# Kernel optimization log

Hardware: AMD Instinct MI355X
Metric: run time of the kernel (lower is better)

Reference implementation:

```python
import jax, jax.numpy as jnp
import numpy as np

T, H = 2048, 1024
NH, NKV, HD = 8, 2, 128
E, TOPK, NG, TKG = 16, 4, 4, 2
F, FS = 1024, 1024
EPS = 1e-6
ROUTED_SCALE = 2.0
THETA = 10000.0


def _rmsnorm(x, w):
    return x * jax.lax.rsqrt(jnp.mean(x * x, axis=-1, keepdims=True) + EPS) * w


def setup_inputs() -> dict:
    key = jax.random.key(0)
    ks = jax.random.split(key, 12)
    s = 0.02
    return {
        "hidden_states": jax.random.normal(ks[0], (T, H), jnp.float32),
        "residual": jax.random.normal(ks[1], (T, H), jnp.float32),
        "position_ids": jnp.arange(T, dtype=jnp.int32),
        "ln1_w": jnp.ones((H,), jnp.float32),
        "qkv_w": s * jax.random.normal(ks[2], (H, (NH + 2 * NKV) * HD), jnp.float32),
        "qnorm_w": jnp.ones((HD,), jnp.float32),
        "knorm_w": jnp.ones((HD,), jnp.float32),
        "dense_w": s * jax.random.normal(ks[3], (NH * HD, H), jnp.float32),
        "ln2_w": jnp.ones((H,), jnp.float32),
        "gate_w": s * jax.random.normal(ks[4], (H, E), jnp.float32),
        "expert_bias": 0.1 * jax.random.normal(ks[5], (E,), jnp.float32),
        "w13": s * jax.random.normal(ks[6], (E, H, 2 * F), jnp.float32),
        "w2": s * jax.random.normal(ks[7], (E, F, H), jnp.float32),
        "ws_gate_up": s * jax.random.normal(ks[8], (H, 2 * FS), jnp.float32),
        "ws_down": s * jax.random.normal(ks[9], (FS, H), jnp.float32),
    }


def block_forward(hidden_states, residual, position_ids, ln1_w, qkv_w, qnorm_w,
                  knorm_w, dense_w, ln2_w, gate_w, expert_bias, w13, w2,
                  ws_gate_up, ws_down):
    # fused add + RMSNorm (input_layernorm with residual)
    resid = hidden_states + residual
    h = _rmsnorm(resid, ln1_w)

    # --- attention ---
    qkv = h @ qkv_w  # [T, (NH+2*NKV)*HD]
    q = qkv[:, : NH * HD].reshape(T, NH, HD)
    k = qkv[:, NH * HD : (NH + NKV) * HD].reshape(T, NKV, HD)
    v = qkv[:, (NH + NKV) * HD :].reshape(T, NKV, HD)
    q = _rmsnorm(q, qnorm_w)  # qk-norm per head_dim
    k = _rmsnorm(k, knorm_w)

    # neox-style RoPE over full head_dim
    inv_freq = 1.0 / (THETA ** (jnp.arange(0, HD, 2, dtype=jnp.float32) / HD))
    ang = position_ids.astype(jnp.float32)[:, None] * inv_freq[None, :]  # [T, HD/2]
    cos = jnp.cos(ang)[:, None, :]
    sin = jnp.sin(ang)[:, None, :]

    def rope(x):
        x1, x2 = x[..., : HD // 2], x[..., HD // 2 :]
        return jnp.concatenate([x1 * cos - x2 * sin, x2 * cos + x1 * sin], axis=-1)

    q, k = rope(q), rope(k)
    rep = NH // NKV
    kr = jnp.repeat(k, rep, axis=1)  # [T, NH, HD]
    vr = jnp.repeat(v, rep, axis=1)

    scores = jnp.einsum("qhd,khd->hqk", q, kr) * (HD ** -0.5)
    causal = jnp.tril(jnp.ones((T, T), bool))
    scores = jnp.where(causal[None], scores, jnp.finfo(scores.dtype).min)
    probs = jax.nn.softmax(scores, axis=-1)
    ctx = jnp.einsum("hqk,khd->qhd", probs, vr).reshape(T, NH * HD)
    attn_out = ctx @ dense_w

    # fused add + RMSNorm (post_attention_layernorm)
    resid2 = attn_out + resid
    h2 = _rmsnorm(resid2, ln2_w)

    # --- MoE router: sigmoid scoring + correction bias, grouped top-k ---
    logits = h2.astype(jnp.float32) @ gate_w  # router in fp32
    s_scores = jax.nn.sigmoid(logits)  # [T, E]
    sfc = s_scores + expert_bias[None, :]
    gview = sfc.reshape(T, NG, E // NG)
    gscores = jax.lax.top_k(gview, 2)[0].sum(-1)  # sum of top-2 per group
    gidx = jax.lax.top_k(gscores, TKG)[1]  # [T, TKG]
    gmask = jax.nn.one_hot(gidx, NG, dtype=sfc.dtype).sum(1)  # [T, NG]
    smask = jnp.repeat(gmask, E // NG, axis=1)  # [T, E]
    masked = jnp.where(smask > 0, sfc, -jnp.inf)
    topk_idx = jax.lax.top_k(masked, TOPK)[1]  # [T, TOPK]
    topk_w = jnp.take_along_axis(s_scores, topk_idx, axis=1)  # weights w/o bias
    topk_w = topk_w / (topk_w.sum(-1, keepdims=True) + 1e-20)  # renormalize
    combine = (jax.nn.one_hot(topk_idx, E, dtype=topk_w.dtype) * topk_w[..., None]).sum(1)  # [T, E]

    # routed experts (dense-over-experts reference for the grouped GEMM)
    gu = jnp.einsum("th,ehf->tef", h2, w13)  # [T, E, 2F]
    g, u = gu[..., :F], gu[..., F:]
    act = jax.nn.silu(g) * u
    y = jnp.einsum("tef,efh->teh", act, w2)
    routed = jnp.einsum("teh,te->th", y, combine) * ROUTED_SCALE

    # shared expert (SwiGLU MLP)
    su = h2 @ ws_gate_up
    shared = (jax.nn.silu(su[:, :FS]) * su[:, FS:]) @ ws_down

    mlp_out = routed + shared
    return mlp_out, resid2


def reference(hidden_states, residual, position_ids, ln1_w, qkv_w, qnorm_w,
              knorm_w, dense_w, ln2_w, gate_w, expert_bias, w13, w2,
              ws_gate_up, ws_down):
    return block_forward(hidden_states, residual, position_ids, ln1_w, qkv_w,
                         qnorm_w, knorm_w, dense_w, ln2_w, gate_w, expert_bias,
                         w13, w2, ws_gate_up, ws_down)
```

## Files before the change

kernel.cpp:

```cpp
#include <hip/hip_runtime.h>
#include <hip/hip_bf16.h>


#define T_TOK 2048
#define H_DIM 1024
#define NHEAD 8
#define NKVH 2
#define HDIM 128
#define QKV_DIM 1536
#define E_EXP 16
#define TOPKE 4
#define F_DIM 1024
#define FS_DIM 1024
#define NPAIR (T_TOK*TOPKE)
#define EPS_F 1e-6f

#define DEV __device__ __forceinline__

typedef __attribute__((ext_vector_type(4))) float f32x4;
typedef __attribute__((ext_vector_type(8))) short s16x8;

DEV float us2f(unsigned short u){ return __uint_as_float(((unsigned int)u)<<16); }
DEV unsigned short f2us(float f){
  __hip_bfloat16 b = __float2bfloat16(f);
  unsigned short u; __builtin_memcpy(&u,&b,2); return u;
}

DEV void gl2lds16(const void* g, void* l){
  __builtin_amdgcn_global_load_lds(
      (const __attribute__((address_space(1))) void*)g,
      (__attribute__((address_space(3))) void*)l, 16, 0, 0);
}

DEV float bred_sum(float v, float* sm){
  #pragma unroll
  for(int o=32;o>0;o>>=1) v += __shfl_down(v,o);
  int w = threadIdx.x>>6, l = threadIdx.x&63;
  __syncthreads();
  if(l==0) sm[w]=v;
  __syncthreads();
  return sm[0]+sm[1]+sm[2]+sm[3];
}

__global__ __launch_bounds__(256) void k_cvt_t(const float* __restrict__ in,
    unsigned short* __restrict__ out, int Kd, int Nd){
  const int z = blockIdx.z;
  const int kb = blockIdx.y*32, nb = blockIdx.x*32;
  __shared__ float Lt[32][33];
  const int tid = threadIdx.x;
  const int r = tid>>3, c4 = (tid&7)*4;
  const float* src = in + (long long)z*Kd*Nd + (long long)(kb+r)*Nd + nb + c4;
  float4 v = *(const float4*)src;
  Lt[r][c4+0]=v.x; Lt[r][c4+1]=v.y; Lt[r][c4+2]=v.z; Lt[r][c4+3]=v.w;
  __syncthreads();
  ushort4 o;
  o.x = f2us(Lt[c4+0][r]); o.y = f2us(Lt[c4+1][r]);
  o.z = f2us(Lt[c4+2][r]); o.w = f2us(Lt[c4+3][r]);
  *(ushort4*)(out + (long long)z*Nd*Kd + (long long)(nb+r)*Kd + kb + c4) = o;
}

template<bool GROUPED, bool GATHER>
__global__ __launch_bounds__(256) void gemm_mfma(
    const unsigned short* __restrict__ A, int lda,
    const unsigned short* __restrict__ Bt, int ldbt, long long bstride,
    unsigned short* __restrict__ C, int ldc,
    const int* __restrict__ rowidx, const int* __restrict__ grpoff,
    int Mdense, int K){
  const int z = blockIdx.z;
  const int rb = GROUPED ? grpoff[z] : 0;
  const int re = GROUPED ? grpoff[z+1] : Mdense;
  const int m0 = rb + blockIdx.y*128;
  if(m0 >= re) return;
  const int n0 = blockIdx.x*128;
  const unsigned short* Bz = Bt + (long long)z*bstride;

  __shared__ unsigned short As[128][32];
  __shared__ unsigned short Bs[128][32];

  const int tid = threadIdx.x;
  const int s0 = tid, s1 = tid+256;
  int gr0 = m0 + (s0>>2), gr1 = m0 + (s1>>2);
  if(GROUPED){ gr0 = min(gr0, re-1); gr1 = min(gr1, re-1); }
  if(GATHER){ gr0 = rowidx[gr0]; gr1 = rowidx[gr1]; }
  const unsigned short* ag0 = A + (long long)gr0*lda + (s0&3)*8;
  const unsigned short* ag1 = A + (long long)gr1*lda + (s1&3)*8;
  const unsigned short* bg0 = Bz + (long long)(n0 + (s0>>2))*ldbt + (s0&3)*8;
  const unsigned short* bg1 = Bz + (long long)(n0 + (s1>>2))*ldbt + (s1&3)*8;
  char* asb = (char*)&As[0][0];
  char* bsb = (char*)&Bs[0][0];
  const int wb = (tid & 192)*16;

  const int w = tid>>6, lane = tid&63;
  const int wm = (w>>1)*64, wn = (w&1)*64;
  const int fr = lane&15, q8 = (lane>>4)*8;

  f32x4 zero = {0.f,0.f,0.f,0.f};
  f32x4 acc[4][4];
  #pragma unroll
  for(int mi=0;mi<4;mi++)
    #pragma unroll
    for(int ni=0;ni<4;ni++) acc[mi][ni]=zero;

  for(int k0=0;k0<K;k0+=32){
    __syncthreads();
    gl2lds16(ag0 + k0, asb + wb);
    gl2lds16(ag1 + k0, asb + 4096 + wb);
    gl2lds16(bg0 + k0, bsb + wb);
    gl2lds16(bg1 + k0, bsb + 4096 + wb);
    __syncthreads();
    s16x8 af[4], bf[4];
    #pragma unroll
    for(int mi=0;mi<4;mi++) af[mi] = *(const s16x8*)&As[wm+mi*16+fr][q8];
    #pragma unroll
    for(int ni=0;ni<4;ni++) bf[ni] = *(const s16x8*)&Bs[wn+ni*16+fr][q8];
    #pragma unroll
    for(int mi=0;mi<4;mi++)
      #pragma unroll
      for(int ni=0;ni<4;ni++)
        acc[mi][ni] = __builtin_amdgcn_mfma_f32_16x16x32_bf16(af[mi], bf[ni], acc[mi][ni], 0,0,0);
  }
  const int q4 = (lane>>4)*4;
  #pragma unroll
  for(int mi=0;mi<4;mi++)
    #pragma unroll
    for(int ni=0;ni<4;ni++){
      const int col = n0 + wn + ni*16 + fr;
      #pragma unroll
      for(int r=0;r<4;r++){
        const int row = m0 + wm + mi*16 + q4 + r;
        if(row < re) C[(long long)row*ldc + col] = f2us(acc[mi][ni][r]);
      }
    }
}

__global__ __launch_bounds__(256) void k_silu(const unsigned short* __restrict__ gu,
    unsigned short* __restrict__ act){
  const int r = blockIdx.x, c = threadIdx.x*4;
  const ushort4 g4 = *(const ushort4*)(gu + (long long)r*2048 + c);
  const ushort4 u4 = *(const ushort4*)(gu + (long long)r*2048 + 1024 + c);
  float g[4] = {us2f(g4.x),us2f(g4.y),us2f(g4.z),us2f(g4.w)};
  float u[4] = {us2f(u4.x),us2f(u4.y),us2f(u4.z),us2f(u4.w)};
  ushort4 o;
  o.x = f2us((g[0]/(1.f+__expf(-g[0])))*u[0]);
  o.y = f2us((g[1]/(1.f+__expf(-g[1])))*u[1]);
  o.z = f2us((g[2]/(1.f+__expf(-g[2])))*u[2]);
  o.w = f2us((g[3]/(1.f+__expf(-g[3])))*u[3]);
  *(ushort4*)(act + (long long)r*1024 + c) = o;
}

__global__ __launch_bounds__(256) void k_add_rmsnorm(const float* __restrict__ hs,
    const float* __restrict__ rs, const float* __restrict__ w,
    float* __restrict__ resid, float* __restrict__ h){
  int t = blockIdx.x, tid = threadIdx.x;
  __shared__ float sm[4];
  const long base = (long)t*H_DIM;
  float x[4]; float ss = 0.f;
  #pragma unroll
  for(int i=0;i<4;i++){
    int c = tid + i*256;
    float v = hs[base+c] + rs[base+c];
    x[i]=v; resid[base+c]=v; ss += v*v;
  }
  float tot = bred_sum(ss, sm);
  float rms = rsqrtf(tot/(float)H_DIM + EPS_F);
  #pragma unroll
  for(int i=0;i<4;i++){
    int c = tid + i*256;
    h[base+c] = x[i]*rms*w[c];
  }
}

template<int EPI_ADD>
__global__ __launch_bounds__(256) void gemm_f32(
    const float* __restrict__ A, int lda,
    const float* __restrict__ B, int ldb,
    float* __restrict__ C, int ldc,
    const float* __restrict__ D, int M, int K){
  const int m0 = blockIdx.y*128;
  const int n0 = blockIdx.x*64;
  __shared__ float As[16][132];
  __shared__ float Bs[16][65];
  float acc[8][4];
  #pragma unroll
  for(int i=0;i<8;i++)
    #pragma unroll
    for(int j=0;j<4;j++) acc[i][j]=0.f;
  const int tid = threadIdx.x;
  const int tx = tid & 15, ty = tid >> 4;
  const int ar = tid >> 1, ac = (tid & 1)*8;
  const int brr = tid >> 4, bc = (tid & 15)*4;
  const float* Aptr = A + (long long)(m0+ar)*lda;
  for(int k0=0;k0<K;k0+=16){
    float4 a0 = *(const float4*)(Aptr + k0 + ac);
    float4 a1 = *(const float4*)(Aptr + k0 + ac + 4);
    float4 bv = *(const float4*)(B + (long long)(k0+brr)*ldb + n0 + bc);
    __syncthreads();
    As[ac+0][ar]=a0.x; As[ac+1][ar]=a0.y; As[ac+2][ar]=a0.z; As[ac+3][ar]=a0.w;
    As[ac+4][ar]=a1.x; As[ac+5][ar]=a1.y; As[ac+6][ar]=a1.z; As[ac+7][ar]=a1.w;
    Bs[brr][bc+0]=bv.x; Bs[brr][bc+1]=bv.y; Bs[brr][bc+2]=bv.z; Bs[brr][bc+3]=bv.w;
    __syncthreads();
    #pragma unroll
    for(int kk=0;kk<16;kk++){
      float a[8], b[4];
      #pragma unroll
      for(int i=0;i<8;i++) a[i]=As[kk][ty*8+i];
      #pragma unroll
      for(int j=0;j<4;j++) b[j]=Bs[kk][tx*4+j];
      #pragma unroll
      for(int i=0;i<8;i++)
        #pragma unroll
        for(int j=0;j<4;j++) acc[i][j] = fmaf(a[i], b[j], acc[i][j]);
    }
  }
  #pragma unroll
  for(int i=0;i<8;i++){
    int r = m0 + ty*8 + i;
    float* crow = C + (long long)r*ldc + n0 + tx*4;
    float4 v = make_float4(acc[i][0],acc[i][1],acc[i][2],acc[i][3]);
    if(EPI_ADD){
      const float4 d = *(const float4*)(D + (long long)r*ldc + n0 + tx*4);
      v.x+=d.x; v.y+=d.y; v.z+=d.z; v.w+=d.w;
    }
    *(float4*)crow = v;
  }
}

__global__ __launch_bounds__(64) void k_qkv_post(const float* __restrict__ qkv,
    const float* __restrict__ qw, const float* __restrict__ kw,
    const int* __restrict__ pos,
    float* __restrict__ qb, float* __restrict__ kb, float* __restrict__ vb){
  int slot = blockIdx.x, t = blockIdx.y, lane = threadIdx.x;
  const float* x = qkv + (long long)t*QKV_DIM + slot*HDIM;
  float x0 = x[lane], x1 = x[lane+64];
  if(slot < 10){
    float ss = x0*x0 + x1*x1;
    #pragma unroll
    for(int o=32;o>0;o>>=1) ss += __shfl_xor(ss,o);
    float rms = rsqrtf(ss/(float)HDIM + EPS_F);
    const float* w = (slot<8)? qw : kw;
    float n0 = x0*rms*w[lane];
    float n1 = x1*rms*w[lane+64];
    float p = (float)pos[t];
    float invf = __expf(-((float)lane/64.f)*9.210340371976184f);
    float ang = p*invf;
    float s = sinf(ang), c = cosf(ang);
    float o0 = n0*c - n1*s;
    float o1 = n1*c + n0*s;
    float* dst = (slot<8)? (qb + ((long long)slot*T_TOK + t)*HDIM)
                         : (kb + ((long long)(slot-8)*T_TOK + t)*HDIM);
    dst[lane]=o0; dst[lane+64]=o1;
  } else {
    float* dst = vb + ((long long)(slot-10)*T_TOK + t)*HDIM;
    dst[lane]=x0; dst[lane+64]=x1;
  }
}

#define FBQ 32
#define FBK 64
__global__ __launch_bounds__(256,2) void k_flash(const float* __restrict__ qb,
    const float* __restrict__ kb, const float* __restrict__ vb,
    float* __restrict__ ctx){
  const int h = blockIdx.x;
  const int by = blockIdx.y;
  const int qt = (by < 32) ? (63 - by) : (by - 32);
  const int kv = h >> 2;
  const int q0 = qt * FBQ;
  const int tid = threadIdx.x;
  const int tx = tid & 15, ty = tid >> 4;
  __shared__ float Qs[HDIM][32];
  __shared__ float Ks[HDIM][64];
  __shared__ float Vs[FBK][HDIM];
  const float scale = 0.08838834764831845f;

  {
    int r = tid>>3, cb = (tid&7)*16;
    const float* src = qb + ((long long)h*T_TOK + q0 + r)*HDIM + cb;
    #pragma unroll
    for(int j=0;j<4;j++){
      float4 v4 = *(const float4*)(src + j*4);
      Qs[cb+j*4+0][r]=v4.x; Qs[cb+j*4+1][r]=v4.y;
      Qs[cb+j*4+2][r]=v4.z; Qs[cb+j*4+3][r]=v4.w;
    }
  }

  float m0=-1e30f, m1=-1e30f, l0=0.f, l1=0.f;
  float O0[8], O1[8];
  #pragma unroll
  for(int j=0;j<8;j++){ O0[j]=0.f; O1[j]=0.f; }

  const int nkt = (qt>>1) + 1;
  const float* kbase = kb + (long long)kv*T_TOK*HDIM;
  const float* vbase = vb + (long long)kv*T_TOK*HDIM;
  const int lbase = tid & 48;

  for(int kt=0; kt<nkt; kt++){
    const int k0 = kt*FBK;
    __syncthreads();
    {
      int r = tid>>2, cb = (tid&3)*32;
      const float* ks = kbase + (long long)(k0+r)*HDIM + cb;
      #pragma unroll
      for(int j=0;j<8;j++){
        float4 v4 = *(const float4*)(ks + j*4);
        Ks[cb+j*4+0][r]=v4.x; Ks[cb+j*4+1][r]=v4.y;
        Ks[cb+j*4+2][r]=v4.z; Ks[cb+j*4+3][r]=v4.w;
      }
      #pragma unroll
      for(int j=0;j<8;j++){
        int idx = tid + 256*j;
        int vr = idx>>5, dc = (idx&31)*4;
        *(float4*)&Vs[vr][dc] = *(const float4*)(vbase + (long long)(k0+vr)*HDIM + dc);
      }
    }
    __syncthreads();

    float s00=0,s01=0,s02=0,s03=0, s10=0,s11=0,s12=0,s13=0;
    const float* qsp = &Qs[0][ty*2];
    const float* ksp = &Ks[0][tx*4];
    #pragma unroll 8
    for(int kk=0;kk<HDIM;kk++){
      float2 q2 = *(const float2*)(qsp + kk*32);
      float4 k4 = *(const float4*)(ksp + kk*64);
      s00=fmaf(q2.x,k4.x,s00); s01=fmaf(q2.x,k4.y,s01);
      s02=fmaf(q2.x,k4.z,s02); s03=fmaf(q2.x,k4.w,s03);
      s10=fmaf(q2.y,k4.x,s10); s11=fmaf(q2.y,k4.y,s11);
      s12=fmaf(q2.y,k4.z,s12); s13=fmaf(q2.y,k4.w,s13);
    }
    float p0[4] = {s00*scale, s01*scale, s02*scale, s03*scale};
    float p1[4] = {s10*scale, s11*scale, s12*scale, s13*scale};
    if(kt == nkt-1){
      #pragma unroll
      for(int ci=0;ci<4;ci++){
        int c = k0 + tx*4 + ci;
        if(c > q0 + ty*2)     p0[ci] = -1e30f;
        if(c > q0 + ty*2 + 1) p1[ci] = -1e30f;
      }
    }
    float rm0 = fmaxf(fmaxf(p0[0],p0[1]),fmaxf(p0[2],p0[3]));
    float rm1 = fmaxf(fmaxf(p1[0],p1[1]),fmaxf(p1[2],p1[3]));
    #pragma unroll
    for(int o=1;o<16;o<<=1){
      rm0 = fmaxf(rm0, __shfl_xor(rm0,o));
      rm1 = fmaxf(rm1, __shfl_xor(rm1,o));
    }
    float mn0 = fmaxf(m0,rm0), mn1 = fmaxf(m1,rm1);
    float a0 = __expf(m0-mn0), a1 = __expf(m1-mn1);
    float rs0=0.f, rs1=0.f;
    #pragma unroll
    for(int ci=0;ci<4;ci++){
      p0[ci] = __expf(p0[ci]-mn0); rs0 += p0[ci];
      p1[ci] = __expf(p1[ci]-mn1); rs1 += p1[ci];
    }
    #pragma unroll
    for(int o=1;o<16;o<<=1){
      rs0 += __shfl_xor(rs0,o);
      rs1 += __shfl_xor(rs1,o);
    }
    l0 = l0*a0 + rs0; l1 = l1*a1 + rs1;
    m0 = mn0; m1 = mn1;
    #pragma unroll
    for(int j=0;j<8;j++){ O0[j]*=a0; O1[j]*=a1; }

    #pragma unroll 4
    for(int kc=0;kc<16;kc++){
      float pa[4], pb[4];
      #pragma unroll
      for(int ki=0;ki<4;ki++){
        pa[ki] = __shfl(p0[ki], lbase + kc);
        pb[ki] = __shfl(p1[ki], lbase + kc);
      }
      #pragma unroll
      for(int ki=0;ki<4;ki++){
        const float* vrow = &Vs[kc*4+ki][0];
        float4 va  = *(const float4*)(vrow + tx*4);
        float4 vb4 = *(const float4*)(vrow + 64 + tx*4);
        float qa = pa[ki], qb2 = pb[ki];
        O0[0]=fmaf(qa,va.x,O0[0]);  O0[1]=fmaf(qa,va.y,O0[1]);
        O0[2]=fmaf(qa,va.z,O0[2]);  O0[3]=fmaf(qa,va.w,O0[3]);
        O0[4]=fmaf(qa,vb4.x,O0[4]); O0[5]=fmaf(qa,vb4.y,O0[5]);
        O0[6]=fmaf(qa,vb4.z,O0[6]); O0[7]=fmaf(qa,vb4.w,O0[7]);
        O1[0]=fmaf(qb2,va.x,O1[0]);  O1[1]=fmaf(qb2,va.y,O1[1]);
        O1[2]=fmaf(qb2,va.z,O1[2]);  O1[3]=fmaf(qb2,va.w,O1[3]);
        O1[4]=fmaf(qb2,vb4.x,O1[4]); O1[5]=fmaf(qb2,vb4.y,O1[5]);
        O1[6]=fmaf(qb2,vb4.z,O1[6]); O1[7]=fmaf(qb2,vb4.w,O1[7]);
      }
    }
  }
  float inv0 = 1.f/l0, inv1 = 1.f/l1;
  float* dst0 = ctx + (long long)(q0 + ty*2)*(NHEAD*HDIM) + h*HDIM + tx*4;
  float* dst1 = dst0 + NHEAD*HDIM;
  *(float4*)dst0      = make_float4(O0[0]*inv0,O0[1]*inv0,O0[2]*inv0,O0[3]*inv0);
  *(float4*)(dst0+64) = make_float4(O0[4]*inv0,O0[5]*inv0,O0[6]*inv0,O0[7]*inv0);
  *(float4*)dst1      = make_float4(O1[0]*inv1,O1[1]*inv1,O1[2]*inv1,O1[3]*inv1);
  *(float4*)(dst1+64) = make_float4(O1[4]*inv1,O1[5]*inv1,O1[6]*inv1,O1[7]*inv1);
}

__global__ __launch_bounds__(256) void k_rms2(const float* __restrict__ r2,
    const float* __restrict__ w, float* __restrict__ h2f,
    unsigned short* __restrict__ h2b){
  int t = blockIdx.x, tid = threadIdx.x;
  __shared__ float sm[4];
  const long base = (long)t*H_DIM;
  float x[4]; float ss=0.f;
  #pragma unroll
  for(int i=0;i<4;i++){
    int c = tid+i*256;
    float v = r2[base+c];
    x[i]=v; ss += v*v;
  }
  float tot = bred_sum(ss, sm);
  float rms = rsqrtf(tot/(float)H_DIM + EPS_F);
  #pragma unroll
  for(int i=0;i<4;i++){
    int c = tid+i*256;
    float v = x[i]*rms*w[c];
    h2f[base+c] = v;
    h2b[base+c] = f2us(v);
  }
}

__global__ __launch_bounds__(256) void k_router(const float* __restrict__ h2,
    const float* __restrict__ gw, const float* __restrict__ eb,
    int* __restrict__ topk_idx, float* __restrict__ topk_w, int* __restrict__ counts){
  int t = blockIdx.x, tid = threadIdx.x;
  int e = tid & 15, seg = tid >> 4;
  const float* hrow = h2 + (long long)t*H_DIM;
  float part = 0.f;
  #pragma unroll 4
  for(int i=0;i<64;i++){
    int hh = seg*64 + i;
    part += hrow[hh]*gw[hh*E_EXP + e];
  }
  __shared__ float pm[16][17];
  __shared__ float sS[16], sfc[16];
  pm[seg][e] = part;
  __syncthreads();
  if(tid < 16){
    float l = 0.f;
    #pragma unroll
    for(int s=0;s<16;s++) l += pm[s][tid];
    float sg = 1.f/(1.f+expf(-l));
    sS[tid]=sg; sfc[tid]=sg+eb[tid];
  }
  __syncthreads();
  if(tid==0){
    float gs[4];
    #pragma unroll
    for(int g=0; g<4; g++){
      float m1=-1e30f, m2=-1e30f;
      for(int j=0;j<4;j++){
        float v=sfc[g*4+j];
        if(v>m1){ m2=m1; m1=v; } else if(v>m2){ m2=v; }
      }
      gs[g]=m1+m2;
    }
    int g1=0; for(int g=1;g<4;g++) if(gs[g]>gs[g1]) g1=g;
    int g2=-1; for(int g=0;g<4;g++){ if(g==g1) continue; if(g2<0||gs[g]>gs[g2]) g2=g; }
    bool taken[16];
    #pragma unroll
    for(int i=0;i<16;i++) taken[i]=false;
    int idx[4];
    for(int j=0;j<4;j++){
      int best=-1; float bv=-1e30f;
      for(int i=0;i<16;i++){
        int g=i>>2;
        if(g!=g1 && g!=g2) continue;
        if(taken[i]) continue;
        if(best<0 || sfc[i]>bv){ best=i; bv=sfc[i]; }
      }
      taken[best]=true; idx[j]=best;
    }
    float w[4]; float s=0.f;
    #pragma unroll
    for(int j=0;j<4;j++){ w[j]=sS[idx[j]]; s+=w[j]; }
    s += 1e-20f;
    #pragma unroll
    for(int j=0;j<4;j++){
      topk_idx[t*4+j]=idx[j];
      topk_w[t*4+j]=w[j]/s;
      atomicAdd(&counts[idx[j]],1);
    }
  }
}

__global__ void k_zero(int* __restrict__ counts){ if(threadIdx.x<16) counts[threadIdx.x]=0; }

__global__ void k_scan(const int* __restrict__ counts, int* __restrict__ offs, int* __restrict__ cursor){
  if(threadIdx.x==0){
    int s=0;
    for(int e2=0;e2<16;e2++){ offs[e2]=s; cursor[e2]=s; s+=counts[e2]; }
    offs[16]=s;
  }
}

__global__ __launch_bounds__(256) void k_scatter(const int* __restrict__ topk_idx,
    int* __restrict__ cursor, int* __restrict__ pair_tok, int* __restrict__ tok2pair){
  int i = blockIdx.x*256 + threadIdx.x;
  int e = topk_idx[i];
  int pos = atomicAdd(&cursor[e],1);
  pair_tok[pos] = i>>2;
  tok2pair[i] = pos;
}

__global__ __launch_bounds__(256) void k_combine(const unsigned short* __restrict__ y,
    const unsigned short* __restrict__ sout, const int* __restrict__ tok2pair,
    const float* __restrict__ topk_w, float* __restrict__ out0){
  int t = blockIdx.x, tid = threadIdx.x;
  int p[4]; float w[4];
  #pragma unroll
  for(int j=0;j<4;j++){ p[j]=tok2pair[t*4+j]; w[j]=topk_w[t*4+j]*2.0f; }
  const long base = (long)t*H_DIM;
  #pragma unroll
  for(int i=0;i<4;i++){
    int c = tid + i*256;
    float v = us2f(sout[base+c]);
    #pragma unroll
    for(int j=0;j<4;j++) v += w[j]*us2f(y[(long long)p[j]*H_DIM + c]);
    out0[base+c] = v;
  }
}

extern "C" void kernel_launch(void* const* d_in, const int* in_sizes, int n_in,
                              void* d_out, int out_size, void* d_ws, size_t ws_size,
                              hipStream_t stream) {
  const float* hs   = (const float*)d_in[0];
  const float* rsd  = (const float*)d_in[1];
  const int*   pos  = (const int*)d_in[2];
  const float* ln1  = (const float*)d_in[3];
  const float* qkvw = (const float*)d_in[4];
  const float* qnw  = (const float*)d_in[5];
  const float* knw  = (const float*)d_in[6];
  const float* dw   = (const float*)d_in[7];
  const float* ln2  = (const float*)d_in[8];
  const float* gw   = (const float*)d_in[9];
  const float* eb   = (const float*)d_in[10];
  const float* w13  = (const float*)d_in[11];
  const float* w2   = (const float*)d_in[12];
  const float* wsgu = (const float*)d_in[13];
  const float* wsd  = (const float*)d_in[14];
  float* out0 = (float*)d_out;
  float* out1 = out0 + (size_t)T_TOK*H_DIM;

  char* W = (char*)d_ws;
  float* resid = (float*)(W + 0);
  float* h     = (float*)(W + 8388608);
  float* ctx   = h;
  float* qkv   = (float*)(W + 16777216);
  float* qb    = (float*)(W + 29360128);
  float* h2f   = (float*)(W + 37748736);
  float* kb    = (float*)(W + 46137344);
  float* vb    = (float*)(W + 48234496);
  unsigned short* gu    = (unsigned short*)(W + 8388608);
  unsigned short* ybuf  = (unsigned short*)(W + 8388608);
  unsigned short* sgu   = (unsigned short*)(W + 16777216);
  unsigned short* sact  = (unsigned short*)(W + 0);
  unsigned short* sout  = (unsigned short*)(W + 46137344);
  unsigned short* h2b   = (unsigned short*)(W + 50331648);
  unsigned short* act   = (unsigned short*)(W + 54525952);
  unsigned short* w13t  = (unsigned short*)(W + 71303168);
  unsigned short* w2t   = (unsigned short*)(W + 138412032);
  unsigned short* wsgut = (unsigned short*)(W + 171966464);
  unsigned short* wsdt  = (unsigned short*)(W + 176160768);
  float* topkw = (float*)(W + 178257920);
  int* topki   = (int*)(W + 178290688);
  int* ptok    = (int*)(W + 178323456);
  int* t2p     = (int*)(W + 178356224);
  int* cnt     = (int*)(W + 178388992);
  int* offs    = (int*)(W + 178389056);
  int* cur     = (int*)(W + 178389184);

  k_cvt_t<<<dim3(64,32,16), 256, 0, stream>>>(w13,  w13t,  1024, 2048);
  k_cvt_t<<<dim3(32,32,16), 256, 0, stream>>>(w2,   w2t,   1024, 1024);
  k_cvt_t<<<dim3(64,32,1),  256, 0, stream>>>(wsgu, wsgut, 1024, 2048);
  k_cvt_t<<<dim3(32,32,1),  256, 0, stream>>>(wsd,  wsdt,  1024, 1024);
  k_add_rmsnorm<<<T_TOK, 256, 0, stream>>>(hs, rsd, ln1, resid, h);
  gemm_f32<0><<<dim3(QKV_DIM/64, T_TOK/128), 256, 0, stream>>>(
      h, H_DIM, qkvw, QKV_DIM, qkv, QKV_DIM, nullptr, T_TOK, H_DIM);
  k_qkv_post<<<dim3(12, T_TOK), 64, 0, stream>>>(qkv, qnw, knw, pos, qb, kb, vb);
  k_flash<<<dim3(NHEAD, 64), 256, 0, stream>>>(qb, kb, vb, ctx);
  gemm_f32<1><<<dim3(H_DIM/64, T_TOK/128), 256, 0, stream>>>(
      ctx, NHEAD*HDIM, dw, H_DIM, out1, H_DIM, resid, T_TOK, NHEAD*HDIM);
  k_rms2<<<T_TOK, 256, 0, stream>>>(out1, ln2, h2f, h2b);
  k_zero<<<1, 64, 0, stream>>>(cnt);
  k_router<<<T_TOK, 256, 0, stream>>>(h2f, gw, eb, topki, topkw, cnt);
  k_scan<<<1, 64, 0, stream>>>(cnt, offs, cur);
  k_scatter<<<NPAIR/256, 256, 0, stream>>>(topki, cur, ptok, t2p);
  gemm_mfma<false,false><<<dim3(16,16,1), 256, 0, stream>>>(
      h2b, 1024, wsgut, 1024, 0, sgu, 2048, nullptr, nullptr, T_TOK, 1024);
  k_silu<<<T_TOK, 256, 0, stream>>>(sgu, sact);
  gemm_mfma<false,false><<<dim3(8,16,1), 256, 0, stream>>>(
      sact, 1024, wsdt, 1024, 0, sout, 1024, nullptr, nullptr, T_TOK, 1024);
  gemm_mfma<true,true><<<dim3(16,64,16), 256, 0, stream>>>(
      h2b, 1024, w13t, 1024, (long long)2048*1024, gu, 2048, ptok, offs, 0, 1024);
  k_silu<<<NPAIR, 256, 0, stream>>>(gu, act);
  gemm_mfma<true,false><<<dim3(8,64,16), 256, 0, stream>>>(
      act, 1024, w2t, 1024, (long long)1024*1024, ybuf, 1024, nullptr, offs, 0, 1024);
  k_combine<<<T_TOK, 256, 0, stream>>>(ybuf, sout, t2p, topkw, out0);
}
```

Measured before the change: 1.107 ms.

## Restructure flash attention with 128-key tiles, swizzled async K staging, LDS-staged probabilities

Rewrites the causal attention kernel to process 128-key tiles, halving the outer iteration count. Each thread now computes a 4x4 score tile. K is staged into a swizzled shared-memory buffer with direct global-to-LDS copies. Q and V are read straight from global memory through the cache instead of shared memory. The softmax probabilities are written to a swizzled LDS region that reuses the tail of the K buffer, replacing the cross-lane shuffle broadcast. This aims to cut shuffle and LDS transpose overhead, at the cost of more global/L2 traffic for Q and V, a larger 64KB shared-memory footprint, and extra barriers.

After: 1.120 ms. Within noise of the previous version (+1.2%).

```diff
diff --git a/kernel.cpp b/kernel.cpp
--- a/kernel.cpp
+++ b/kernel.cpp
@@ -256,7 +256,7 @@
 }
 
 #define FBQ 32
-#define FBK 64
+#define FBK 128
 __global__ __launch_bounds__(256,2) void k_flash(const float* __restrict__ qb,
     const float* __restrict__ kb, const float* __restrict__ vb,
     float* __restrict__ ctx){
@@ -266,133 +266,145 @@
   const int kv = h >> 2;
   const int q0 = qt * FBQ;
   const int tid = threadIdx.x;
-  const int tx = tid & 15, ty = tid >> 4;
-  __shared__ float Qs[HDIM][32];
-  __shared__ float Ks[HDIM][64];
-  __shared__ float Vs[FBK][HDIM];
+  const int lane = tid & 63;
+  const int w = tid >> 6;
+  const int tx = tid & 31;
+  const int ty = tid >> 5;
+  const int fsw = tx & 7;
+
+  __shared__ float4 smem4[4096];
+  char*  smem = (char*)smem4;
+  float* Ksf  = (float*)smem;
+  float* Psf  = (float*)(smem + 49152);
+
   const float scale = 0.08838834764831845f;
-
-  {
-    int r = tid>>3, cb = (tid&7)*16;
-    const float* src = qb + ((long long)h*T_TOK + q0 + r)*HDIM + cb;
-    #pragma unroll
-    for(int j=0;j<4;j++){
-      float4 v4 = *(const float4*)(src + j*4);
-      Qs[cb+j*4+0][r]=v4.x; Qs[cb+j*4+1][r]=v4.y;
-      Qs[cb+j*4+2][r]=v4.z; Qs[cb+j*4+3][r]=v4.w;
-    }
-  }
-
-  float m0=-1e30f, m1=-1e30f, l0=0.f, l1=0.f;
-  float O0[8], O1[8];
-  #pragma unroll
-  for(int j=0;j<8;j++){ O0[j]=0.f; O1[j]=0.f; }
-
-  const int nkt = (qt>>1) + 1;
   const float* kbase = kb + (long long)kv*T_TOK*HDIM;
   const float* vbase = vb + (long long)kv*T_TOK*HDIM;
-  const int lbase = tid & 48;
+  const float* qrow0 = qb + ((long long)h*T_TOK + q0 + ty*4)*HDIM;
+
+  float m_[4], l_[4], O[4][4];
+  #pragma unroll
+  for(int qi=0;qi<4;qi++){
+    m_[qi] = -1e30f; l_[qi] = 0.f;
+    #pragma unroll
+    for(int j=0;j<4;j++) O[qi][j] = 0.f;
+  }
+
+  const int nkt = (qt >> 2) + 1;
 
   for(int kt=0; kt<nkt; kt++){
-    const int k0 = kt*FBK;
+    const int k0 = kt * FBK;
     __syncthreads();
     {
-      int r = tid>>2, cb = (tid&3)*32;
-      const float* ks = kbase + (long long)(k0+r)*HDIM + cb;
-      #pragma unroll
-      for(int j=0;j<8;j++){
-        float4 v4 = *(const float4*)(ks + j*4);
-        Ks[cb+j*4+0][r]=v4.x; Ks[cb+j*4+1][r]=v4.y;
-        Ks[cb+j*4+2][r]=v4.z; Ks[cb+j*4+3][r]=v4.w;
+      const float* kcur = kbase + (long long)k0*HDIM;
+      #pragma unroll
+      for(int i=0;i<16;i++){
+        const int rbase = (w<<5) + (i<<1);
+        const int f = (i>>1) & 7;
+        const float* src = kcur + (long long)(rbase + (lane>>5))*HDIM
+                                + (((lane&31)^f)<<2);
+        gl2lds16(src, smem + rbase*512);
       }
-      #pragma unroll
-      for(int j=0;j<8;j++){
-        int idx = tid + 256*j;
-        int vr = idx>>5, dc = (idx&31)*4;
-        *(float4*)&Vs[vr][dc] = *(const float4*)(vbase + (long long)(k0+vr)*HDIM + dc);
+    }
+    __syncthreads();
+
+    float s[4][4];
+    #pragma unroll
+    for(int qi=0;qi<4;qi++)
+      #pragma unroll
+      for(int ki=0;ki<4;ki++) s[qi][ki] = 0.f;
+
+    #pragma unroll 2
+    for(int dc=0; dc<32; dc++){
+      float4 qv[4];
+      #pragma unroll
+      for(int qi=0;qi<4;qi++) qv[qi] = *(const float4*)(qrow0 + qi*HDIM + dc*4);
+      float4 kf[4];
+      #pragma unroll
+      for(int ki=0;ki<4;ki++)
+        kf[ki] = *(const float4*)&Ksf[(size_t)(4*tx+ki)*128 + ((dc ^ fsw)<<2)];
+      #pragma unroll
+      for(int qi=0;qi<4;qi++)
+        #pragma unroll
+        for(int ki=0;ki<4;ki++){
+          s[qi][ki] = fmaf(qv[qi].x, kf[ki].x, s[qi][ki]);
+          s[qi][ki] = fmaf(qv[qi].y, kf[ki].y, s[qi][ki]);
+          s[qi][ki] = fmaf(qv[qi].z, kf[ki].z, s[qi][ki]);
+          s[qi][ki] = fmaf(qv[qi].w, kf[ki].w, s[qi][ki]);
+        }
+    }
+
+    const bool last = (kt == nkt-1);
+    float rm[4];
+    #pragma unroll
+    for(int qi=0;qi<4;qi++){
+      #pragma unroll
+      for(int ki=0;ki<4;ki++){
+        float v = s[qi][ki]*scale;
+        if(last && (k0 + 4*tx + ki > q0 + ty*4 + qi)) v = -1e30f;
+        s[qi][ki] = v;
       }
-    }
-    __syncthreads();
-
-    float s00=0,s01=0,s02=0,s03=0, s10=0,s11=0,s12=0,s13=0;
-    const float* qsp = &Qs[0][ty*2];
-    const float* ksp = &Ks[0][tx*4];
-    #pragma unroll 8
-    for(int kk=0;kk<HDIM;kk++){
-      float2 q2 = *(const float2*)(qsp + kk*32);
-      float4 k4 = *(const float4*)(ksp + kk*64);
-      s00=fmaf(q2.x,k4.x,s00); s01=fmaf(q2.x,k4.y,s01);
-      s02=fmaf(q2.x,k4.z,s02); s03=fmaf(q2.x,k4.w,s03);
-      s10=fmaf(q2.y,k4.x,s10); s11=fmaf(q2.y,k4.y,s11);
-      s12=fmaf(q2.y,k4.z,s12); s13=fmaf(q2.y,k4.w,s13);
-    }
-    float p0[4] = {s00*scale, s01*scale, s02*scale, s03*scale};
-    float p1[4] = {s10*scale, s11*scale, s12*scale, s13*scale};
-    if(kt == nkt-1){
-      #pragma unroll
-      for(int ci=0;ci<4;ci++){
-        int c = k0 + tx*4 + ci;
-        if(c > q0 + ty*2)     p0[ci] = -1e30f;
-        if(c > q0 + ty*2 + 1) p1[ci] = -1e30f;
-      }
-    }
-    float rm0 = fmaxf(fmaxf(p0[0],p0[1]),fmaxf(p0[2],p0[3]));
-    float rm1 = fmaxf(fmaxf(p1[0],p1[1]),fmaxf(p1[2],p1[3]));
-    #pragma unroll
-    for(int o=1;o<16;o<<=1){
-      rm0 = fmaxf(rm0, __shfl_xor(rm0,o));
-      rm1 = fmaxf(rm1, __shfl_xor(rm1,o));
-    }
-    float mn0 = fmaxf(m0,rm0), mn1 = fmaxf(m1,rm1);
-    float a0 = __expf(m0-mn0), a1 = __expf(m1-mn1);
-    float rs0=0.f, rs1=0.f;
-    #pragma unroll
-    for(int ci=0;ci<4;ci++){
-      p0[ci] = __expf(p0[ci]-mn0); rs0 += p0[ci];
-      p1[ci] = __expf(p1[ci]-mn1); rs1 += p1[ci];
-    }
-    #pragma unroll
-    for(int o=1;o<16;o<<=1){
-      rs0 += __shfl_xor(rs0,o);
-      rs1 += __shfl_xor(rs1,o);
-    }
-    l0 = l0*a0 + rs0; l1 = l1*a1 + rs1;
-    m0 = mn0; m1 = mn1;
-    #pragma unroll
-    for(int j=0;j<8;j++){ O0[j]*=a0; O1[j]*=a1; }
-
+      rm[qi] = fmaxf(fmaxf(s[qi][0],s[qi][1]), fmaxf(s[qi][2],s[qi][3]));
+    }
+    #pragma unroll
+    for(int o=1;o<32;o<<=1){
+      #pragma unroll
+      for(int qi=0;qi<4;qi++) rm[qi] = fmaxf(rm[qi], __shfl_xor(rm[qi], o));
+    }
+    float a_[4], rs[4];
+    #pragma unroll
+    for(int qi=0;qi<4;qi++){
+      float mn = fmaxf(m_[qi], rm[qi]);
+      a_[qi] = __expf(m_[qi] - mn);
+      m_[qi] = mn;
+      float r = 0.f;
+      #pragma unroll
+      for(int ki=0;ki<4;ki++){ s[qi][ki] = __expf(s[qi][ki] - mn); r += s[qi][ki]; }
+      rs[qi] = r;
+    }
+    #pragma unroll
+    for(int o=1;o<32;o<<=1){
+      #pragma unroll
+      for(int qi=0;qi<4;qi++) rs[qi] += __shfl_xor(rs[qi], o);
+    }
+    #pragma unroll
+    for(int qi=0;qi<4;qi++){
+      l_[qi] = l_[qi]*a_[qi] + rs[qi];
+      #pragma unroll
+      for(int j=0;j<4;j++) O[qi][j] *= a_[qi];
+    }
+
+    __syncthreads();
+    #pragma unroll
+    for(int ki=0;ki<4;ki++){
+      float4 pv;
+      pv.x = s[0][ki]; pv.y = s[1][ki]; pv.z = s[2][ki]; pv.w = s[3][ki];
+      *(float4*)&Psf[(size_t)(4*tx+ki)*32 + ((ty ^ fsw)<<2)] = pv;
+    }
+    __syncthreads();
+
+    const float* vcur = vbase + (long long)k0*HDIM + tx*4;
     #pragma unroll 4
-    for(int kc=0;kc<16;kc++){
-      float pa[4], pb[4];
-      #pragma unroll
-      for(int ki=0;ki<4;ki++){
-        pa[ki] = __shfl(p0[ki], lbase + kc);
-        pb[ki] = __shfl(p1[ki], lbase + kc);
-      }
-      #pragma unroll
-      for(int ki=0;ki<4;ki++){
-        const float* vrow = &Vs[kc*4+ki][0];
-        float4 va  = *(const float4*)(vrow + tx*4);
-        float4 vb4 = *(const float4*)(vrow + 64 + tx*4);
-        float qa = pa[ki], qb2 = pb[ki];
-        O0[0]=fmaf(qa,va.x,O0[0]);  O0[1]=fmaf(qa,va.y,O0[1]);
-        O0[2]=fmaf(qa,va.z,O0[2]);  O0[3]=fmaf(qa,va.w,O0[3]);
-        O0[4]=fmaf(qa,vb4.x,O0[4]); O0[5]=fmaf(qa,vb4.y,O0[5]);
-        O0[6]=fmaf(qa,vb4.z,O0[6]); O0[7]=fmaf(qa,vb4.w,O0[7]);
-        O1[0]=fmaf(qb2,va.x,O1[0]);  O1[1]=fmaf(qb2,va.y,O1[1]);
-        O1[2]=fmaf(qb2,va.z,O1[2]);  O1[3]=fmaf(qb2,va.w,O1[3]);
-        O1[4]=fmaf(qb2,vb4.x,O1[4]); O1[5]=fmaf(qb2,vb4.y,O1[5]);
-        O1[6]=fmaf(qb2,vb4.z,O1[6]); O1[7]=fmaf(qb2,vb4.w,O1[7]);
-      }
-    }
-  }
-  float inv0 = 1.f/l0, inv1 = 1.f/l1;
-  float* dst0 = ctx + (long long)(q0 + ty*2)*(NHEAD*HDIM) + h*HDIM + tx*4;
-  float* dst1 = dst0 + NHEAD*HDIM;
-  *(float4*)dst0      = make_float4(O0[0]*inv0,O0[1]*inv0,O0[2]*inv0,O0[3]*inv0);
-  *(float4*)(dst0+64) = make_float4(O0[4]*inv0,O0[5]*inv0,O0[6]*inv0,O0[7]*inv0);
-  *(float4*)dst1      = make_float4(O1[0]*inv1,O1[1]*inv1,O1[2]*inv1,O1[3]*inv1);
-  *(float4*)(dst1+64) = make_float4(O1[4]*inv1,O1[5]*inv1,O1[6]*inv1,O1[7]*inv1);
+    for(int k=0;k<FBK;k++){
+      float4 p4 = *(const float4*)&Psf[(size_t)k*32 + ((ty ^ ((k>>2)&7))<<2)];
+      float4 vv = *(const float4*)(vcur + (size_t)k*HDIM);
+      O[0][0]=fmaf(p4.x,vv.x,O[0][0]); O[0][1]=fmaf(p4.x,vv.y,O[0][1]);
+      O[0][2]=fmaf(p4.x,vv.z,O[0][2]); O[0][3]=fmaf(p4.x,vv.w,O[0][3]);
+      O[1][0]=fmaf(p4.y,vv.x,O[1][0]); O[1][1]=fmaf(p4.y,vv.y,O[1][1]);
+      O[1][2]=fmaf(p4.y,vv.z,O[1][2]); O[1][3]=fmaf(p4.y,vv.w,O[1][3]);
+      O[2][0]=fmaf(p4.z,vv.x,O[2][0]); O[2][1]=fmaf(p4.z,vv.y,O[2][1]);
+      O[2][2]=fmaf(p4.z,vv.z,O[2][2]); O[2][3]=fmaf(p4.z,vv.w,O[2][3]);
+      O[3][0]=fmaf(p4.w,vv.x,O[3][0]); O[3][1]=fmaf(p4.w,vv.y,O[3][1]);
+      O[3][2]=fmaf(p4.w,vv.z,O[3][2]); O[3][3]=fmaf(p4.w,vv.w,O[3][3]);
+    }
+  }
+
+  #pragma unroll
+  for(int qi=0;qi<4;qi++){
+    float inv = 1.f/l_[qi];
+    float4 o4 = make_float4(O[qi][0]*inv, O[qi][1]*inv, O[qi][2]*inv, O[qi][3]*inv);
+    *(float4*)(ctx + (long long)(q0 + ty*4 + qi)*(NHEAD*HDIM) + h*HDIM + tx*4) = o4;
+  }
 }
 
 __global__ __launch_bounds__(256) void k_rms2(const float* __restrict__ r2,
```
